# Kernel tuning notes

Measured on AMD Instinct MI355X. Metric: run time of the kernel, lower is better.

Reference implementation:

```python
import jax, jax.numpy as jnp
import numpy as np

B, T, R, D = 32, 128, 49, 512
H_EXP, H_CLS = 256, 256
THRES = 0.1
LAM = 4.0
NEG_INF = -1e9


def setup_inputs() -> dict:
    key = jax.random.key(0)
    ks = jax.random.split(key, 16)
    s = 0.02
    return {
        "word_emb": jax.random.normal(ks[0], (B, T, D), jnp.float32),
        "region_emb": jax.random.normal(ks[1], (B, R, D), jnp.float32),
        "attention_mask": jnp.ones((B, T), jnp.int32),
        # pos expert MLP: D -> H_EXP -> 1
        "pw1": jax.random.normal(ks[2], (D, H_EXP), jnp.float32) * s,
        "pb1": jnp.zeros((H_EXP,), jnp.float32),
        "pw2": jax.random.normal(ks[3], (H_EXP, 1), jnp.float32) * s,
        "pb2": jnp.zeros((1,), jnp.float32),
        # neg expert MLP: D -> H_EXP -> 1
        "nw1": jax.random.normal(ks[4], (D, H_EXP), jnp.float32) * s,
        "nb1": jnp.zeros((H_EXP,), jnp.float32),
        "nw2": jax.random.normal(ks[5], (H_EXP, 1), jnp.float32) * s,
        "nb2": jnp.zeros((1,), jnp.float32),
        # fc: D -> 1
        "fcw": jax.random.normal(ks[6], (D, 1), jnp.float32) * s,
        "fcb": jnp.zeros((1,), jnp.float32),
        # classifier: D -> H_CLS -> 2 (dropout is eval-mode identity)
        "cw1": jax.random.normal(ks[7], (D, H_CLS), jnp.float32) * s,
        "cb1": jnp.zeros((H_CLS,), jnp.float32),
        "cw2": jax.random.normal(ks[8], (H_CLS, 2), jnp.float32) * s,
        "cb2": jnp.zeros((2,), jnp.float32),
    }


def _mlp_score(x, w1, b1, w2, b2):
    # sigmoid(Linear(tanh(Linear(x)))) -> squeeze last dim
    return jax.nn.sigmoid(jnp.tanh(x @ w1 + b1) @ w2 + b2)[..., 0]


def reference(word_emb, region_emb, attention_mask,
              pw1, pb1, pw2, pb2, nw1, nb1, nw2, nb2,
              fcw, fcb, cw1, cb1, cw2, cb2):
    mask_f = attention_mask.astype(word_emb.dtype)  # [B,T]

    # cross attention word x region: [B,T,R]
    attn = jnp.einsum("btd,brd->btr", word_emb, region_emb)
    attn_neg = (attn - THRES > 0).astype(attn.dtype)  # [B,T,R]
    attn_pos = jax.nn.softmax(
        jnp.where(attn_neg > 0, attn, NEG_INF) * LAM, axis=-1)
    pos = jnp.einsum("btr,brd->btd", attn_pos, region_emb) + word_emb

    # pos expert: sigmoid score, zeroed where token has no positive region
    # or is padding (padding tokens were excluded by the ragged gather).
    expert_neg_mask = attn_neg.sum(-1) == 0  # [B,T] bool
    pos_score = _mlp_score(pos, pw1, pb1, pw2, pb2)  # [B,T]
    pos_score = jnp.where(expert_neg_mask, 0.0, pos_score) * mask_f
    pos_score = jax.nn.relu(pos_score)
    pos_agg = jnp.einsum("bt,btd->bd", pos_score, pos)

    # neg expert over all (token, region) pair embeddings, masked to the
    # ragged set neg_mask = (1 - attn_neg) * attention_mask
    all_emb = word_emb[:, :, None, :] + region_emb[:, None, :, :]  # [B,T,R,D]
    neg_mask = (1.0 - attn_neg) * mask_f[:, :, None]  # [B,T,R]
    neg_score = _mlp_score(all_emb, nw1, nb1, nw2, nb2)  # [B,T,R]
    neg_score = jax.nn.relu(neg_score * neg_mask)
    neg_agg = jnp.einsum("btr,btrd->bd", neg_score, all_emb)

    result = jnp.stack([neg_agg, pos_agg], axis=1)  # [B,2,D]

    choose = (result @ fcw + fcb)[..., 0]  # [B,2]
    choose_mask = attn_neg.sum(axis=(-1, -2)) == 0  # [B]
    choose = choose.at[:, 0].set(
        jnp.where(choose_mask, NEG_INF, choose[:, 0]))
    path_prob = jax.nn.softmax(choose, axis=-1)  # [B,2]
    final = jnp.einsum("bk,bkd->bd", path_prob, result)  # [B,D]

    logits = jax.nn.relu(final @ cw1 + cb1) @ cw2 + cb2  # [B,2]
    return (logits, path_prob)
```

## Files before the change

### kernel.cpp

```cpp
#include <hip/hip_runtime.h>

#define B_ 32
#define T_ 128
#define R_ 49
#define D_ 512
#define HE_ 256
#define HC_ 256

#define NG_GEMM1 354
#define NG_K1 512
#define NG_GEMM2 256
#define NG_NEGB 512

typedef float f32x4 __attribute__((ext_vector_type(4)));
typedef short s16x8 __attribute__((ext_vector_type(8)));
typedef short s16x4 __attribute__((ext_vector_type(4)));

__device__ __forceinline__ unsigned short bf16rne(float f) {
  unsigned u = __float_as_uint(f);
  u += 0x7FFF + ((u >> 16) & 1);
  return (unsigned short)(u >> 16);
}
__device__ __forceinline__ float rcp_fast(float x) {
  return __builtin_amdgcn_rcpf(x);
}
__device__ __forceinline__ float tanh_fast(float x) {
  float e = __expf(2.0f * x);
  return fmaf(-2.0f, rcp_fast(e + 1.0f), 1.0f);
}
__device__ __forceinline__ float sigmoid_fast(float x) {
  return rcp_fast(1.0f + __expf(-x));
}
__device__ __forceinline__ float wave_sum(float v) {
#pragma unroll
  for (int off = 32; off; off >>= 1) v += __shfl_down(v, off);
  return v;
}

__global__ __launch_bounds__(256) void pack_w(
    const float* __restrict__ nw1, const float* __restrict__ pw1,
    unsigned short* __restrict__ wp, float* __restrict__ nsr) {
  int gid = blockIdx.x * 256 + threadIdx.x;
  if (gid < B_ * R_) nsr[gid] = 0.f;
  int mat = gid >> 14;
  int rem = gid & 16383;
  int lane = rem & 63;
  int tile = rem >> 6;
  int kt = tile >> 4, ct = tile & 15;
  const float* W = mat ? pw1 : nw1;
  int k0 = kt * 32 + (lane >> 4) * 8;
  int c = ct * 16 + (lane & 15);
  s16x8 pk;
#pragma unroll
  for (int j = 0; j < 8; ++j)
    pk[j] = (short)bf16rne(W[(size_t)(k0 + j) * HE_ + c]);
  *(s16x8*)(wp + (size_t)gid * 8) = pk;
}

__global__ __launch_bounds__(512) void m1_gemm_k1(
    const float* __restrict__ word, const float* __restrict__ region,
    const unsigned short* __restrict__ wpack, const float* __restrict__ nb1,
    const int* __restrict__ amask, float* __restrict__ wh,
    float* __restrict__ rh, float* __restrict__ pos,
    float* __restrict__ negcnt, unsigned long long* __restrict__ nmask) {
  __shared__ alignas(16) unsigned short As[16 * 512];
  __shared__ float attn_s[8][52];
  __shared__ alignas(16) float wp_T[49][8];
  int tid = threadIdx.x, wave = tid >> 6, lane = tid & 63;
  int bid = blockIdx.x;

  if (bid < NG_GEMM1) {
    const float* A;
    float* outp;
    int row0;
    bool useb;
    if (bid < 256) {
      A = word; outp = wh; row0 = bid * 16; useb = true;
    } else {
      A = region; outp = rh; row0 = (bid - 256) * 16; useb = false;
    }
    const float4* A4 = (const float4*)(A + (size_t)row0 * D_);
#pragma unroll
    for (int it = 0; it < 4; ++it) {
      int f = it * 512 + tid;
      int row = f >> 7, kq = f & 127;
      float4 v = A4[f];
      int bo = (row * 1024 + kq * 8) ^ ((row & 7) << 4);
      s16x4 pk;
      pk[0] = (short)bf16rne(v.x);
      pk[1] = (short)bf16rne(v.y);
      pk[2] = (short)bf16rne(v.z);
      pk[3] = (short)bf16rne(v.w);
      *(s16x4*)((char*)As + bo) = pk;
    }
    __syncthreads();
    int rl = lane & 15, kg = lane >> 4;
    f32x4 acc0 = {0.f, 0.f, 0.f, 0.f}, acc1 = {0.f, 0.f, 0.f, 0.f};
    const s16x8* Wp8 = (const s16x8*)wpack;
    int ct0 = wave, ct1 = wave + 8;
#pragma unroll
    for (int kt = 0; kt < 16; ++kt) {
      int bo = (rl * 1024 + kt * 64 + kg * 16) ^ ((rl & 7) << 4);
      s16x8 af = *(const s16x8*)((char*)As + bo);
      s16x8 b0 = Wp8[(size_t)(kt * 16 + ct0) * 64 + lane];
      s16x8 b1 = Wp8[(size_t)(kt * 16 + ct1) * 64 + lane];
      acc0 = __builtin_amdgcn_mfma_f32_16x16x32_bf16(af, b0, acc0, 0, 0, 0);
      acc1 = __builtin_amdgcn_mfma_f32_16x16x32_bf16(af, b1, acc1, 0, 0, 0);
    }
    float bb0 = useb ? nb1[ct0 * 16 + rl] : 0.f;
    float bb1 = useb ? nb1[ct1 * 16 + rl] : 0.f;
    int r0 = row0 + kg * 4;
#pragma unroll
    for (int q = 0; q < 4; ++q) {
      outp[(size_t)(r0 + q) * HE_ + ct0 * 16 + rl] = acc0[q] + bb0;
      outp[(size_t)(r0 + q) * HE_ + ct1 * 16 + rl] = acc1[q] + bb1;
    }
    return;
  }

  int bid2 = bid - NG_GEMM1;
  int b = bid2 >> 4;
  int t0 = (bid2 & 15) * 8;
  int bt0 = b * T_ + t0;
  const float* reg = region + (size_t)b * R_ * D_;

  const float4* word4 = (const float4*)word;
  float4 wv[8][2];
#pragma unroll
  for (int t = 0; t < 8; ++t)
#pragma unroll
    for (int j = 0; j < 2; ++j)
      wv[t][j] = word4[(size_t)(bt0 + t) * 128 + lane * 2 + j];

  for (int r = wave; r < R_; r += 8) {
    const float4* rrow4 = (const float4*)(reg + (size_t)r * D_);
    float4 rv0 = rrow4[lane * 2 + 0];
    float4 rv1 = rrow4[lane * 2 + 1];
#pragma unroll
    for (int t = 0; t < 8; ++t) {
      float4 w0 = wv[t][0], w1 = wv[t][1];
      float acc = 0.f;
      acc = fmaf(w0.x, rv0.x, acc);
      acc = fmaf(w0.y, rv0.y, acc);
      acc = fmaf(w0.z, rv0.z, acc);
      acc = fmaf(w0.w, rv0.w, acc);
      acc = fmaf(w1.x, rv1.x, acc);
      acc = fmaf(w1.y, rv1.y, acc);
      acc = fmaf(w1.z, rv1.z, acc);
      acc = fmaf(w1.w, rv1.w, acc);
      acc = wave_sum(acc);
      if (lane == 0) attn_s[t][r] = acc;
    }
  }
  __syncthreads();

  {
    int t = wave;
    int am = amask[bt0 + t];
    float a = (lane < R_) ? attn_s[t][lane] : 0.f;
    float neg = (lane < R_ && (a - 0.1f) > 0.f) ? 1.f : 0.f;
    float masked = (lane < R_) ? ((neg > 0.f) ? a * 4.0f : -4e9f) : -3.0e38f;
    float cnt = wave_sum(neg);
    float m = masked;
#pragma unroll
    for (int off = 32; off; off >>= 1) m = fmaxf(m, __shfl_down(m, off));
    m = __shfl(m, 0);
    float e = (lane < R_) ? __expf(masked - m) : 0.f;
    float s = wave_sum(e);
    s = __shfl(s, 0);
    if (lane < R_) wp_T[lane][t] = e / s;
    bool want = (lane < R_) && (neg == 0.f) && (am != 0);
    unsigned long long bm = __ballot(want);
    if (lane == 0) {
      negcnt[bt0 + t] = cnt;
      nmask[bt0 + t] = bm;
    }
  }
  __syncthreads();

  int d = tid;
  float accs[8] = {0.f, 0.f, 0.f, 0.f, 0.f, 0.f, 0.f, 0.f};
#pragma unroll 7
  for (int r = 0; r < R_; ++r) {
    float g = reg[(size_t)r * D_ + d];
    float4 w0 = *(const float4*)&wp_T[r][0];
    float4 w1 = *(const float4*)&wp_T[r][4];
    accs[0] = fmaf(w0.x, g, accs[0]);
    accs[1] = fmaf(w0.y, g, accs[1]);
    accs[2] = fmaf(w0.z, g, accs[2]);
    accs[3] = fmaf(w0.w, g, accs[3]);
    accs[4] = fmaf(w1.x, g, accs[4]);
    accs[5] = fmaf(w1.y, g, accs[5]);
    accs[6] = fmaf(w1.z, g, accs[6]);
    accs[7] = fmaf(w1.w, g, accs[7]);
  }
#pragma unroll
  for (int t = 0; t < 8; ++t) {
    size_t base = (size_t)(bt0 + t) * D_ + d;
    pos[base] = word[base] + accs[t];
  }
}

__global__ __launch_bounds__(512) void m2_hps_neg(
    const float* __restrict__ pos, const unsigned short* __restrict__ wpack,
    const float* __restrict__ pb1, const float* __restrict__ pw2,
    const float* __restrict__ pb2, const float* __restrict__ negcnt,
    const int* __restrict__ amask, const float* __restrict__ wh,
    const float* __restrict__ rh, const float* __restrict__ nw2,
    const float* __restrict__ nb2,
    const unsigned long long* __restrict__ nmask,
    float* __restrict__ pscore, float* __restrict__ nst,
    float* __restrict__ nsr) {
  __shared__ union SM {
    struct G {
      alignas(16) unsigned short As[16 * 512];
      float sred[16][4];
    } g;
    struct N {
      alignas(16) float rh_s[R_ * HE_];
      alignas(16) float wh_s[8 * HE_];
      int plist[400];
      float nst_l[8];
      float nsr_l[52];
      int cnt_s[8];
      int off_s[8];
      int P;
    } n;
  } sm;
  int tid = threadIdx.x, wave = tid >> 6, lane = tid & 63;
  int bid = blockIdx.x;

  if (bid < NG_GEMM2) {
    int row0 = bid * 16;
    const float4* A4 = (const float4*)(pos + (size_t)row0 * D_);
#pragma unroll
    for (int it = 0; it < 4; ++it) {
      int f = it * 512 + tid;
      int row = f >> 7, kq = f & 127;
      float4 v = A4[f];
      int bo = (row * 1024 + kq * 8) ^ ((row & 7) << 4);
      s16x4 pk;
      pk[0] = (short)bf16rne(v.x);
      pk[1] = (short)bf16rne(v.y);
      pk[2] = (short)bf16rne(v.z);
      pk[3] = (short)bf16rne(v.w);
      *(s16x4*)((char*)sm.g.As + bo) = pk;
    }
    __syncthreads();
    int rl = lane & 15, kg = lane >> 4;
    f32x4 acc0 = {0.f, 0.f, 0.f, 0.f}, acc1 = {0.f, 0.f, 0.f, 0.f};
    const s16x8* Wp8 = (const s16x8*)wpack + 16384;
    int ct0 = wave, ct1 = wave + 8;
#pragma unroll
    for (int kt = 0; kt < 16; ++kt) {
      int bo = (rl * 1024 + kt * 64 + kg * 16) ^ ((rl & 7) << 4);
      s16x8 af = *(const s16x8*)((char*)sm.g.As + bo);
      s16x8 b0 = Wp8[(size_t)(kt * 16 + ct0) * 64 + lane];
      s16x8 b1 = Wp8[(size_t)(kt * 16 + ct1) * 64 + lane];
      acc0 = __builtin_amdgcn_mfma_f32_16x16x32_bf16(af, b0, acc0, 0, 0, 0);
      acc1 = __builtin_amdgcn_mfma_f32_16x16x32_bf16(af, b1, acc1, 0, 0, 0);
    }
    __syncthreads();
    float* hp_s = (float*)sm.g.As;
#pragma unroll
    for (int q = 0; q < 4; ++q) {
      hp_s[(kg * 4 + q) * 256 + ct0 * 16 + rl] = acc0[q];
      hp_s[(kg * 4 + q) * 256 + ct1 * 16 + rl] = acc1[q];
    }
    __syncthreads();
    int c = tid & 255, jh = tid >> 8;
    float pb1c = pb1[c], pw2c = pw2[c];
#pragma unroll
    for (int jj = 0; jj < 8; ++jj) {
      int j = jh * 8 + jj;
      float v = tanh_fast(hp_s[j * 256 + c] + pb1c) * pw2c;
      v = wave_sum(v);
      if (lane == 0) sm.g.sred[j][wave & 3] = v;
    }
    __syncthreads();
    if (tid < 16) {
      float s = sm.g.sred[tid][0] + sm.g.sred[tid][1] + sm.g.sred[tid][2] +
                sm.g.sred[tid][3] + pb2[0];
      s = sigmoid_fast(s);
      int row = row0 + tid;
      if (negcnt[row] == 0.f) s = 0.f;
      s *= (float)amask[row];
      pscore[row] = fmaxf(s, 0.f);
    }
    return;
  }

  int nb = bid - NG_GEMM2;
  int b = nb >> 4, t0 = (nb & 15) * 8;
  int bt0 = b * T_ + t0;
  {
    const float4* src = (const float4*)(rh + (size_t)b * R_ * HE_);
    float4* dst = (float4*)sm.n.rh_s;
    for (int i = tid; i < R_ * (HE_ / 4); i += 512) dst[i] = src[i];
    const float4* srcw = (const float4*)(wh + (size_t)bt0 * HE_);
    float4* dstw = (float4*)sm.n.wh_s;
    for (int i = tid; i < 8 * (HE_ / 4); i += 512) dstw[i] = srcw[i];
  }
  if (tid < 8) {
    sm.n.nst_l[tid] = 0.f;
    sm.n.cnt_s[tid] = __popcll(nmask[bt0 + tid]);
  }
  if (tid < R_) sm.n.nsr_l[tid] = 0.f;
  __syncthreads();
  if (tid == 0) {
    int tot = 0;
#pragma unroll
    for (int w = 0; w < 8; ++w) {
      sm.n.off_s[w] = tot;
      tot += sm.n.cnt_s[w];
    }
    sm.n.P = tot;
  }
  __syncthreads();
  {
    unsigned long long mw = nmask[bt0 + wave];
    if (lane < R_ && ((mw >> lane) & 1ull)) {
      int pfx = __popcll(mw & ((1ull << lane) - 1ull));
      sm.n.plist[sm.n.off_s[wave] + pfx] = (wave << 6) | lane;
    }
  }
  __syncthreads();
  int P = sm.n.P;
  int grp = tid >> 4, gl = tid & 15;
  float4 wnr[4];
#pragma unroll
  for (int k = 0; k < 4; ++k)
    wnr[k] = ((const float4*)nw2)[4 * gl + ((gl + k) & 3)];
  float bias = nb2[0];
  for (int i = grp; i < P; i += 32) {
    int tr = sm.n.plist[i];
    int t = tr >> 6, r = tr & 63;
    const float4* wrow = (const float4*)(sm.n.wh_s + t * HE_);
    const float4* rrow = (const float4*)(sm.n.rh_s + r * HE_);
    float acc = 0.f;
#pragma unroll
    for (int k = 0; k < 4; ++k) {
      int c = 4 * gl + ((gl + k) & 3);
      float4 hw = wrow[c];
      float4 hr = rrow[c];
      float4 wn = wnr[k];
      acc = fmaf(tanh_fast(hw.x + hr.x), wn.x, acc);
      acc = fmaf(tanh_fast(hw.y + hr.y), wn.y, acc);
      acc = fmaf(tanh_fast(hw.z + hr.z), wn.z, acc);
      acc = fmaf(tanh_fast(hw.w + hr.w), wn.w, acc);
    }
    acc += __shfl_xor(acc, 1);
    acc += __shfl_xor(acc, 2);
    acc += __shfl_xor(acc, 4);
    acc += __shfl_xor(acc, 8);
    if (gl == 0) {
      float s = sigmoid_fast(acc + bias);
      atomicAdd(&sm.n.nst_l[t], s);
      atomicAdd(&sm.n.nsr_l[r], s);
    }
  }
  __syncthreads();
  if (tid < 8) {
    nst[bt0 + tid] = sm.n.nst_l[tid];
  } else if (tid >= 64 && tid < 64 + R_) {
    atomicAdd(&nsr[b * R_ + (tid - 64)], sm.n.nsr_l[tid - 64]);
  }
}

__global__ __launch_bounds__(512) void k7a_agg(
    const float* __restrict__ word, const float* __restrict__ region,
    const float* __restrict__ pos, const float* __restrict__ pscore,
    const float* __restrict__ nst, const float* __restrict__ nsr,
    float* __restrict__ nagg, float* __restrict__ pagg) {
  int b = blockIdx.x >> 3, dc = blockIdx.x & 7;
  int tid = threadIdx.x;
  int dl = tid & 63, ts = tid >> 6;
  int d = dc * 64 + dl;
  __shared__ float nst_s[T_], psc_s[T_], nsr_s[R_];
  __shared__ float redn[8][64], redp[8][64];
  if (tid < T_) {
    psc_s[tid] = pscore[b * T_ + tid];
    nst_s[tid] = nst[b * T_ + tid];
  } else if (tid < T_ + R_) {
    nsr_s[tid - T_] = nsr[b * R_ + (tid - T_)];
  }
  __syncthreads();
  float na = 0.f, pa = 0.f;
  for (int t = ts; t < T_; t += 8) {
    size_t base = ((size_t)(b * T_ + t)) * D_ + d;
    na = fmaf(nst_s[t], word[base], na);
    pa = fmaf(psc_s[t], pos[base], pa);
  }
  for (int r = ts; r < R_; r += 8)
    na = fmaf(nsr_s[r], region[((size_t)(b * R_ + r)) * D_ + d], na);
  redn[ts][dl] = na;
  redp[ts][dl] = pa;
  __syncthreads();
  if (tid < 64) {
    float s = 0.f;
#pragma unroll
    for (int k = 0; k < 8; ++k) s += redn[k][tid];
    nagg[(size_t)b * D_ + dc * 64 + tid] = s;
  } else if (tid < 128) {
    int l = tid - 64;
    float s = 0.f;
#pragma unroll
    for (int k = 0; k < 8; ++k) s += redp[k][l];
    pagg[(size_t)b * D_ + dc * 64 + l] = s;
  }
}

__global__ __launch_bounds__(256) void k7b_tail(
    const float* __restrict__ nagg, const float* __restrict__ pagg,
    const float* __restrict__ negcnt, const float* __restrict__ fcw,
    const float* __restrict__ fcb, const float* __restrict__ cw1,
    const float* __restrict__ cb1, const float* __restrict__ cw2,
    const float* __restrict__ cb2, float* __restrict__ out) {
  int b = blockIdx.x, tid = threadIdx.x, lane = tid & 63, wave = tid >> 6;
  __shared__ float na_s[D_], pa_s[D_], fin[D_];
  __shared__ float red[8];
  __shared__ float pp0, pp1;
  float cntp = (tid < T_) ? negcnt[b * T_ + tid] : 0.f;
  float cw = wave_sum(cntp);
  if (lane == 0) red[wave] = cw;
  int d0 = tid, d1 = tid + 256;
  float n0 = nagg[(size_t)b * D_ + d0], n1 = nagg[(size_t)b * D_ + d1];
  float p0 = pagg[(size_t)b * D_ + d0], p1 = pagg[(size_t)b * D_ + d1];
  na_s[d0] = n0;
  na_s[d1] = n1;
  pa_s[d0] = p0;
  pa_s[d1] = p1;
  __syncthreads();
  float cnt_total = red[0] + red[1] + red[2] + red[3];
  float f0 = fcw[d0], f1 = fcw[d1];
  float c0p = n0 * f0 + n1 * f1;
  float c1p = p0 * f0 + p1 * f1;
  c0p = wave_sum(c0p);
  c1p = wave_sum(c1p);
  __syncthreads();
  if (lane == 0) { red[wave] = c0p; red[wave + 4] = c1p; }
  __syncthreads();
  if (tid == 0) {
    float c0 = red[0] + red[1] + red[2] + red[3] + fcb[0];
    float c1 = red[4] + red[5] + red[6] + red[7] + fcb[0];
    if (cnt_total == 0.f) c0 = -1e9f;
    float m = fmaxf(c0, c1);
    float e0 = __expf(c0 - m), e1 = __expf(c1 - m);
    float inv = 1.f / (e0 + e1);
    pp0 = e0 * inv;
    pp1 = e1 * inv;
    out[2 * B_ + 2 * b + 0] = pp0;
    out[2 * B_ + 2 * b + 1] = pp1;
  }
  __syncthreads();
  for (int d = tid; d < D_; d += 256) fin[d] = pp0 * na_s[d] + pp1 * pa_s[d];
  __syncthreads();
  float a0 = cb1[tid], a1 = 0.f, a2 = 0.f, a3 = 0.f;
#pragma unroll 4
  for (int d = 0; d < D_; d += 4) {
    a0 = fmaf(fin[d + 0], cw1[(size_t)(d + 0) * HC_ + tid], a0);
    a1 = fmaf(fin[d + 1], cw1[(size_t)(d + 1) * HC_ + tid], a1);
    a2 = fmaf(fin[d + 2], cw1[(size_t)(d + 2) * HC_ + tid], a2);
    a3 = fmaf(fin[d + 3], cw1[(size_t)(d + 3) * HC_ + tid], a3);
  }
  float acc = fmaxf((a0 + a1) + (a2 + a3), 0.f);
  float l0 = acc * cw2[2 * tid + 0];
  float l1 = acc * cw2[2 * tid + 1];
  l0 = wave_sum(l0);
  l1 = wave_sum(l1);
  __syncthreads();
  if (lane == 0) { red[wave] = l0; red[wave + 4] = l1; }
  __syncthreads();
  if (tid == 0) {
    out[2 * b + 0] = red[0] + red[1] + red[2] + red[3] + cb2[0];
    out[2 * b + 1] = red[4] + red[5] + red[6] + red[7] + cb2[1];
  }
}

extern "C" void kernel_launch(void* const* d_in, const int* in_sizes, int n_in,
                              void* d_out, int out_size, void* d_ws,
                              size_t ws_size, hipStream_t stream) {
  const float* word = (const float*)d_in[0];
  const float* region = (const float*)d_in[1];
  const int* amask = (const int*)d_in[2];
  const float* pw1 = (const float*)d_in[3];
  const float* pb1 = (const float*)d_in[4];
  const float* pw2 = (const float*)d_in[5];
  const float* pb2 = (const float*)d_in[6];
  const float* nw1 = (const float*)d_in[7];
  const float* nb1 = (const float*)d_in[8];
  const float* nw2 = (const float*)d_in[9];
  const float* nb2 = (const float*)d_in[10];
  const float* fcw = (const float*)d_in[11];
  const float* fcb = (const float*)d_in[12];
  const float* cw1 = (const float*)d_in[13];
  const float* cb1 = (const float*)d_in[14];
  const float* cw2 = (const float*)d_in[15];
  const float* cb2 = (const float*)d_in[16];
  float* out = (float*)d_out;

  unsigned short* wpack = (unsigned short*)d_ws;
  float* ws = (float*)d_ws + 131072;
  float* pos = ws;
  float* wh = pos + (size_t)B_ * T_ * D_;
  float* rh = wh + (size_t)B_ * T_ * HE_;
  float* nst = rh + (size_t)B_ * R_ * HE_;
  float* nsr = nst + (size_t)B_ * T_;
  float* negcnt = nsr + (size_t)B_ * R_;
  float* pscore = negcnt + B_ * T_;
  float* nagg = pscore + B_ * T_;
  float* pagg = nagg + (size_t)B_ * D_;
  unsigned long long* nmask =
      (unsigned long long*)(pagg + (size_t)B_ * D_);

  pack_w<<<128, 256, 0, stream>>>(nw1, pw1, wpack, nsr);
  m1_gemm_k1<<<NG_GEMM1 + NG_K1, 512, 0, stream>>>(
      word, region, wpack, nb1, amask, wh, rh, pos, negcnt, nmask);
  m2_hps_neg<<<NG_GEMM2 + NG_NEGB, 512, 0, stream>>>(
      pos, wpack, pb1, pw2, pb2, negcnt, amask, wh, rh, nw2, nb2, nmask,
      pscore, nst, nsr);
  k7a_agg<<<B_ * 8, 512, 0, stream>>>(word, region, pos, pscore, nst, nsr,
                                      nagg, pagg);
  k7b_tail<<<B_, 256, 0, stream>>>(nagg, pagg, negcnt, fcw, fcb, cw1, cb1,
                                   cw2, cb2, out);
}
```

Measured before the change: 85.05 us.

## Regroup kernel stages: fuse weight packing with attention, merge all GEMMs

Weight packing moves into the attention kernel as extra blocks, so there is one fewer launch. The word/region GEMMs move out of that kernel and join the pos-expert GEMM in a single gemm_all launch. The neg-expert scoring becomes its own kernel with smaller shared memory: wh rows are no longer staged and are read directly from global, and a launch-bounds hint is added. The attention loop now processes tokens in two passes of 4 to lower register pressure. The kernel count stays the same, but the dependency grouping changes, and the neg expert now reads wh from global memory instead of LDS.

```diff
diff --git a/kernel.cpp b/kernel.cpp
--- a/kernel.cpp
+++ b/kernel.cpp
@@ -7,9 +7,10 @@
 #define HE_ 256
 #define HC_ 256
 
-#define NG_GEMM1 354
+#define NG_PACK 64
 #define NG_K1 512
-#define NG_GEMM2 256
+#define NG_G1 354
+#define NG_G2 256
 #define NG_NEGB 512
 
 typedef float f32x4 __attribute__((ext_vector_type(4)));
@@ -37,119 +38,71 @@
   return v;
 }
 
-__global__ __launch_bounds__(256) void pack_w(
+__global__ __launch_bounds__(512, 8) void k1_pack(
+    const float* __restrict__ word, const float* __restrict__ region,
     const float* __restrict__ nw1, const float* __restrict__ pw1,
-    unsigned short* __restrict__ wp, float* __restrict__ nsr) {
-  int gid = blockIdx.x * 256 + threadIdx.x;
-  if (gid < B_ * R_) nsr[gid] = 0.f;
-  int mat = gid >> 14;
-  int rem = gid & 16383;
-  int lane = rem & 63;
-  int tile = rem >> 6;
-  int kt = tile >> 4, ct = tile & 15;
-  const float* W = mat ? pw1 : nw1;
-  int k0 = kt * 32 + (lane >> 4) * 8;
-  int c = ct * 16 + (lane & 15);
-  s16x8 pk;
-#pragma unroll
-  for (int j = 0; j < 8; ++j)
-    pk[j] = (short)bf16rne(W[(size_t)(k0 + j) * HE_ + c]);
-  *(s16x8*)(wp + (size_t)gid * 8) = pk;
-}
-
-__global__ __launch_bounds__(512) void m1_gemm_k1(
-    const float* __restrict__ word, const float* __restrict__ region,
-    const unsigned short* __restrict__ wpack, const float* __restrict__ nb1,
-    const int* __restrict__ amask, float* __restrict__ wh,
-    float* __restrict__ rh, float* __restrict__ pos,
+    const int* __restrict__ amask, unsigned short* __restrict__ wp,
+    float* __restrict__ nsr, float* __restrict__ pos,
     float* __restrict__ negcnt, unsigned long long* __restrict__ nmask) {
-  __shared__ alignas(16) unsigned short As[16 * 512];
   __shared__ float attn_s[8][52];
   __shared__ alignas(16) float wp_T[49][8];
   int tid = threadIdx.x, wave = tid >> 6, lane = tid & 63;
   int bid = blockIdx.x;
 
-  if (bid < NG_GEMM1) {
-    const float* A;
-    float* outp;
-    int row0;
-    bool useb;
-    if (bid < 256) {
-      A = word; outp = wh; row0 = bid * 16; useb = true;
-    } else {
-      A = region; outp = rh; row0 = (bid - 256) * 16; useb = false;
-    }
-    const float4* A4 = (const float4*)(A + (size_t)row0 * D_);
-#pragma unroll
-    for (int it = 0; it < 4; ++it) {
-      int f = it * 512 + tid;
-      int row = f >> 7, kq = f & 127;
-      float4 v = A4[f];
-      int bo = (row * 1024 + kq * 8) ^ ((row & 7) << 4);
-      s16x4 pk;
-      pk[0] = (short)bf16rne(v.x);
-      pk[1] = (short)bf16rne(v.y);
-      pk[2] = (short)bf16rne(v.z);
-      pk[3] = (short)bf16rne(v.w);
-      *(s16x4*)((char*)As + bo) = pk;
-    }
-    __syncthreads();
-    int rl = lane & 15, kg = lane >> 4;
-    f32x4 acc0 = {0.f, 0.f, 0.f, 0.f}, acc1 = {0.f, 0.f, 0.f, 0.f};
-    const s16x8* Wp8 = (const s16x8*)wpack;
-    int ct0 = wave, ct1 = wave + 8;
-#pragma unroll
-    for (int kt = 0; kt < 16; ++kt) {
-      int bo = (rl * 1024 + kt * 64 + kg * 16) ^ ((rl & 7) << 4);
-      s16x8 af = *(const s16x8*)((char*)As + bo);
-      s16x8 b0 = Wp8[(size_t)(kt * 16 + ct0) * 64 + lane];
-      s16x8 b1 = Wp8[(size_t)(kt * 16 + ct1) * 64 + lane];
-      acc0 = __builtin_amdgcn_mfma_f32_16x16x32_bf16(af, b0, acc0, 0, 0, 0);
-      acc1 = __builtin_amdgcn_mfma_f32_16x16x32_bf16(af, b1, acc1, 0, 0, 0);
-    }
-    float bb0 = useb ? nb1[ct0 * 16 + rl] : 0.f;
-    float bb1 = useb ? nb1[ct1 * 16 + rl] : 0.f;
-    int r0 = row0 + kg * 4;
-#pragma unroll
-    for (int q = 0; q < 4; ++q) {
-      outp[(size_t)(r0 + q) * HE_ + ct0 * 16 + rl] = acc0[q] + bb0;
-      outp[(size_t)(r0 + q) * HE_ + ct1 * 16 + rl] = acc1[q] + bb1;
-    }
+  if (bid < NG_PACK) {
+    int gid = bid * 512 + tid;
+    if (gid < B_ * R_) nsr[gid] = 0.f;
+    int mat = gid >> 14;
+    int rem = gid & 16383;
+    int plane = rem & 63;
+    int tile = rem >> 6;
+    int kt = tile >> 4, ct = tile & 15;
+    const float* W = mat ? pw1 : nw1;
+    int k0 = kt * 32 + (plane >> 4) * 8;
+    int c = ct * 16 + (plane & 15);
+    s16x8 pk;
+#pragma unroll
+    for (int j = 0; j < 8; ++j)
+      pk[j] = (short)bf16rne(W[(size_t)(k0 + j) * HE_ + c]);
+    *(s16x8*)(wp + (size_t)gid * 8) = pk;
     return;
   }
 
-  int bid2 = bid - NG_GEMM1;
+  int bid2 = bid - NG_PACK;
   int b = bid2 >> 4;
   int t0 = (bid2 & 15) * 8;
   int bt0 = b * T_ + t0;
   const float* reg = region + (size_t)b * R_ * D_;
-
   const float4* word4 = (const float4*)word;
-  float4 wv[8][2];
-#pragma unroll
-  for (int t = 0; t < 8; ++t)
-#pragma unroll
-    for (int j = 0; j < 2; ++j)
-      wv[t][j] = word4[(size_t)(bt0 + t) * 128 + lane * 2 + j];
-
-  for (int r = wave; r < R_; r += 8) {
-    const float4* rrow4 = (const float4*)(reg + (size_t)r * D_);
-    float4 rv0 = rrow4[lane * 2 + 0];
-    float4 rv1 = rrow4[lane * 2 + 1];
-#pragma unroll
-    for (int t = 0; t < 8; ++t) {
-      float4 w0 = wv[t][0], w1 = wv[t][1];
-      float acc = 0.f;
-      acc = fmaf(w0.x, rv0.x, acc);
-      acc = fmaf(w0.y, rv0.y, acc);
-      acc = fmaf(w0.z, rv0.z, acc);
-      acc = fmaf(w0.w, rv0.w, acc);
-      acc = fmaf(w1.x, rv1.x, acc);
-      acc = fmaf(w1.y, rv1.y, acc);
-      acc = fmaf(w1.z, rv1.z, acc);
-      acc = fmaf(w1.w, rv1.w, acc);
-      acc = wave_sum(acc);
-      if (lane == 0) attn_s[t][r] = acc;
+
+#pragma unroll
+  for (int pass = 0; pass < 2; ++pass) {
+    int tp = pass * 4;
+    float4 wv[4][2];
+#pragma unroll
+    for (int t = 0; t < 4; ++t)
+#pragma unroll
+      for (int j = 0; j < 2; ++j)
+        wv[t][j] = word4[(size_t)(bt0 + tp + t) * 128 + lane * 2 + j];
+    for (int r = wave; r < R_; r += 8) {
+      const float4* rrow4 = (const float4*)(reg + (size_t)r * D_);
+      float4 rv0 = rrow4[lane * 2 + 0];
+      float4 rv1 = rrow4[lane * 2 + 1];
+#pragma unroll
+      for (int t = 0; t < 4; ++t) {
+        float4 w0 = wv[t][0], w1 = wv[t][1];
+        float acc = 0.f;
+        acc = fmaf(w0.x, rv0.x, acc);
+        acc = fmaf(w0.y, rv0.y, acc);
+        acc = fmaf(w0.z, rv0.z, acc);
+        acc = fmaf(w0.w, rv0.w, acc);
+        acc = fmaf(w1.x, rv1.x, acc);
+        acc = fmaf(w1.y, rv1.y, acc);
+        acc = fmaf(w1.z, rv1.z, acc);
+        acc = fmaf(w1.w, rv1.w, acc);
+        acc = wave_sum(acc);
+        if (lane == 0) attn_s[tp + t][r] = acc;
+      }
     }
   }
   __syncthreads();
@@ -201,131 +154,149 @@
   }
 }
 
-__global__ __launch_bounds__(512) void m2_hps_neg(
+__global__ __launch_bounds__(512) void gemm_all(
+    const float* __restrict__ word, const float* __restrict__ region,
     const float* __restrict__ pos, const unsigned short* __restrict__ wpack,
-    const float* __restrict__ pb1, const float* __restrict__ pw2,
-    const float* __restrict__ pb2, const float* __restrict__ negcnt,
-    const int* __restrict__ amask, const float* __restrict__ wh,
-    const float* __restrict__ rh, const float* __restrict__ nw2,
-    const float* __restrict__ nb2,
-    const unsigned long long* __restrict__ nmask,
-    float* __restrict__ pscore, float* __restrict__ nst,
-    float* __restrict__ nsr) {
-  __shared__ union SM {
-    struct G {
-      alignas(16) unsigned short As[16 * 512];
-      float sred[16][4];
-    } g;
-    struct N {
-      alignas(16) float rh_s[R_ * HE_];
-      alignas(16) float wh_s[8 * HE_];
-      int plist[400];
-      float nst_l[8];
-      float nsr_l[52];
-      int cnt_s[8];
-      int off_s[8];
-      int P;
-    } n;
-  } sm;
+    const float* __restrict__ nb1, const float* __restrict__ pb1,
+    const float* __restrict__ pw2, const float* __restrict__ pb2,
+    const float* __restrict__ negcnt, const int* __restrict__ amask,
+    float* __restrict__ wh, float* __restrict__ rh,
+    float* __restrict__ pscore) {
+  __shared__ alignas(16) unsigned short As[16 * 512];
+  __shared__ float sred[16][4];
   int tid = threadIdx.x, wave = tid >> 6, lane = tid & 63;
   int bid = blockIdx.x;
 
-  if (bid < NG_GEMM2) {
-    int row0 = bid * 16;
-    const float4* A4 = (const float4*)(pos + (size_t)row0 * D_);
-#pragma unroll
-    for (int it = 0; it < 4; ++it) {
-      int f = it * 512 + tid;
-      int row = f >> 7, kq = f & 127;
-      float4 v = A4[f];
-      int bo = (row * 1024 + kq * 8) ^ ((row & 7) << 4);
-      s16x4 pk;
-      pk[0] = (short)bf16rne(v.x);
-      pk[1] = (short)bf16rne(v.y);
-      pk[2] = (short)bf16rne(v.z);
-      pk[3] = (short)bf16rne(v.w);
-      *(s16x4*)((char*)sm.g.As + bo) = pk;
-    }
-    __syncthreads();
-    int rl = lane & 15, kg = lane >> 4;
-    f32x4 acc0 = {0.f, 0.f, 0.f, 0.f}, acc1 = {0.f, 0.f, 0.f, 0.f};
-    const s16x8* Wp8 = (const s16x8*)wpack + 16384;
-    int ct0 = wave, ct1 = wave + 8;
-#pragma unroll
-    for (int kt = 0; kt < 16; ++kt) {
-      int bo = (rl * 1024 + kt * 64 + kg * 16) ^ ((rl & 7) << 4);
-      s16x8 af = *(const s16x8*)((char*)sm.g.As + bo);
-      s16x8 b0 = Wp8[(size_t)(kt * 16 + ct0) * 64 + lane];
-      s16x8 b1 = Wp8[(size_t)(kt * 16 + ct1) * 64 + lane];
-      acc0 = __builtin_amdgcn_mfma_f32_16x16x32_bf16(af, b0, acc0, 0, 0, 0);
-      acc1 = __builtin_amdgcn_mfma_f32_16x16x32_bf16(af, b1, acc1, 0, 0, 0);
-    }
-    __syncthreads();
-    float* hp_s = (float*)sm.g.As;
+  bool isg2 = (bid >= NG_G1);
+  const float* A;
+  float* outp = nullptr;
+  int row0;
+  bool useb = false;
+  const s16x8* Wp8;
+  if (!isg2) {
+    if (bid < 256) {
+      A = word; outp = wh; row0 = bid * 16; useb = true;
+    } else {
+      A = region; outp = rh; row0 = (bid - 256) * 16;
+    }
+    Wp8 = (const s16x8*)wpack;
+  } else {
+    A = pos; row0 = (bid - NG_G1) * 16;
+    Wp8 = (const s16x8*)wpack + 16384;
+  }
+  const float4* A4 = (const float4*)(A + (size_t)row0 * D_);
+#pragma unroll
+  for (int it = 0; it < 4; ++it) {
+    int f = it * 512 + tid;
+    int row = f >> 7, kq = f & 127;
+    float4 v = A4[f];
+    int bo = (row * 1024 + kq * 8) ^ ((row & 7) << 4);
+    s16x4 pk;
+    pk[0] = (short)bf16rne(v.x);
+    pk[1] = (short)bf16rne(v.y);
+    pk[2] = (short)bf16rne(v.z);
+    pk[3] = (short)bf16rne(v.w);
+    *(s16x4*)((char*)As + bo) = pk;
+  }
+  __syncthreads();
+  int rl = lane & 15, kg = lane >> 4;
+  f32x4 acc0 = {0.f, 0.f, 0.f, 0.f}, acc1 = {0.f, 0.f, 0.f, 0.f};
+  int ct0 = wave, ct1 = wave + 8;
+#pragma unroll
+  for (int kt = 0; kt < 16; ++kt) {
+    int bo = (rl * 1024 + kt * 64 + kg * 16) ^ ((rl & 7) << 4);
+    s16x8 af = *(const s16x8*)((char*)As + bo);
+    s16x8 b0 = Wp8[(size_t)(kt * 16 + ct0) * 64 + lane];
+    s16x8 b1 = Wp8[(size_t)(kt * 16 + ct1) * 64 + lane];
+    acc0 = __builtin_amdgcn_mfma_f32_16x16x32_bf16(af, b0, acc0, 0, 0, 0);
+    acc1 = __builtin_amdgcn_mfma_f32_16x16x32_bf16(af, b1, acc1, 0, 0, 0);
+  }
+  if (!isg2) {
+    float bb0 = useb ? nb1[ct0 * 16 + rl] : 0.f;
+    float bb1 = useb ? nb1[ct1 * 16 + rl] : 0.f;
+    int r0 = row0 + kg * 4;
 #pragma unroll
     for (int q = 0; q < 4; ++q) {
-      hp_s[(kg * 4 + q) * 256 + ct0 * 16 + rl] = acc0[q];
-      hp_s[(kg * 4 + q) * 256 + ct1 * 16 + rl] = acc1[q];
-    }
-    __syncthreads();
-    int c = tid & 255, jh = tid >> 8;
-    float pb1c = pb1[c], pw2c = pw2[c];
-#pragma unroll
-    for (int jj = 0; jj < 8; ++jj) {
-      int j = jh * 8 + jj;
-      float v = tanh_fast(hp_s[j * 256 + c] + pb1c) * pw2c;
-      v = wave_sum(v);
-      if (lane == 0) sm.g.sred[j][wave & 3] = v;
-    }
-    __syncthreads();
-    if (tid < 16) {
-      float s = sm.g.sred[tid][0] + sm.g.sred[tid][1] + sm.g.sred[tid][2] +
-                sm.g.sred[tid][3] + pb2[0];
-      s = sigmoid_fast(s);
-      int row = row0 + tid;
-      if (negcnt[row] == 0.f) s = 0.f;
-      s *= (float)amask[row];
-      pscore[row] = fmaxf(s, 0.f);
+      outp[(size_t)(r0 + q) * HE_ + ct0 * 16 + rl] = acc0[q] + bb0;
+      outp[(size_t)(r0 + q) * HE_ + ct1 * 16 + rl] = acc1[q] + bb1;
     }
     return;
   }
-
-  int nb = bid - NG_GEMM2;
+  __syncthreads();
+  float* hp_s = (float*)As;
+#pragma unroll
+  for (int q = 0; q < 4; ++q) {
+    hp_s[(kg * 4 + q) * 256 + ct0 * 16 + rl] = acc0[q];
+    hp_s[(kg * 4 + q) * 256 + ct1 * 16 + rl] = acc1[q];
+  }
+  __syncthreads();
+  int c = tid & 255, jh = tid >> 8;
+  float pb1c = pb1[c], pw2c = pw2[c];
+#pragma unroll
+  for (int jj = 0; jj < 8; ++jj) {
+    int j = jh * 8 + jj;
+    float v = tanh_fast(hp_s[j * 256 + c] + pb1c) * pw2c;
+    v = wave_sum(v);
+    if (lane == 0) sred[j][wave & 3] = v;
+  }
+  __syncthreads();
+  if (tid < 16) {
+    float s = sred[tid][0] + sred[tid][1] + sred[tid][2] + sred[tid][3] +
+              pb2[0];
+    s = sigmoid_fast(s);
+    int row = row0 + tid;
+    if (negcnt[row] == 0.f) s = 0.f;
+    s *= (float)amask[row];
+    pscore[row] = fmaxf(s, 0.f);
+  }
+}
+
+__global__ __launch_bounds__(512, 6) void neg_expert(
+    const float* __restrict__ wh, const float* __restrict__ rh,
+    const float* __restrict__ nw2, const float* __restrict__ nb2,
+    const unsigned long long* __restrict__ nmask, float* __restrict__ nst,
+    float* __restrict__ nsr) {
+  __shared__ alignas(16) float rh_s[R_ * HE_];
+  __shared__ int plist[400];
+  __shared__ float nst_l[8];
+  __shared__ float nsr_l[52];
+  __shared__ int cnt_s[8];
+  __shared__ int off_s[8];
+  __shared__ int P_s;
+  int tid = threadIdx.x, wave = tid >> 6, lane = tid & 63;
+  int nb = blockIdx.x;
   int b = nb >> 4, t0 = (nb & 15) * 8;
   int bt0 = b * T_ + t0;
   {
     const float4* src = (const float4*)(rh + (size_t)b * R_ * HE_);
-    float4* dst = (float4*)sm.n.rh_s;
+    float4* dst = (float4*)rh_s;
     for (int i = tid; i < R_ * (HE_ / 4); i += 512) dst[i] = src[i];
-    const float4* srcw = (const float4*)(wh + (size_t)bt0 * HE_);
-    float4* dstw = (float4*)sm.n.wh_s;
-    for (int i = tid; i < 8 * (HE_ / 4); i += 512) dstw[i] = srcw[i];
   }
   if (tid < 8) {
-    sm.n.nst_l[tid] = 0.f;
-    sm.n.cnt_s[tid] = __popcll(nmask[bt0 + tid]);
-  }
-  if (tid < R_) sm.n.nsr_l[tid] = 0.f;
+    nst_l[tid] = 0.f;
+    cnt_s[tid] = __popcll(nmask[bt0 + tid]);
+  }
+  if (tid < R_) nsr_l[tid] = 0.f;
   __syncthreads();
   if (tid == 0) {
     int tot = 0;
 #pragma unroll
     for (int w = 0; w < 8; ++w) {
-      sm.n.off_s[w] = tot;
-      tot += sm.n.cnt_s[w];
-    }
-    sm.n.P = tot;
+      off_s[w] = tot;
+      tot += cnt_s[w];
+    }
+    P_s = tot;
   }
   __syncthreads();
   {
     unsigned long long mw = nmask[bt0 + wave];
     if (lane < R_ && ((mw >> lane) & 1ull)) {
       int pfx = __popcll(mw & ((1ull << lane) - 1ull));
-      sm.n.plist[sm.n.off_s[wave] + pfx] = (wave << 6) | lane;
-    }
-  }
-  __syncthreads();
-  int P = sm.n.P;
+      plist[off_s[wave] + pfx] = (wave << 6) | lane;
+    }
+  }
+  __syncthreads();
+  int P = P_s;
   int grp = tid >> 4, gl = tid & 15;
   float4 wnr[4];
 #pragma unroll
@@ -333,10 +304,10 @@
     wnr[k] = ((const float4*)nw2)[4 * gl + ((gl + k) & 3)];
   float bias = nb2[0];
   for (int i = grp; i < P; i += 32) {
-    int tr = sm.n.plist[i];
+    int tr = plist[i];
     int t = tr >> 6, r = tr & 63;
-    const float4* wrow = (const float4*)(sm.n.wh_s + t * HE_);
-    const float4* rrow = (const float4*)(sm.n.rh_s + r * HE_);
+    const float4* wrow = (const float4*)(wh + (size_t)(bt0 + t) * HE_);
+    const float4* rrow = (const float4*)(rh_s + r * HE_);
     float acc = 0.f;
 #pragma unroll
     for (int k = 0; k < 4; ++k) {
@@ -355,15 +326,15 @@
     acc += __shfl_xor(acc, 8);
     if (gl == 0) {
       float s = sigmoid_fast(acc + bias);
-      atomicAdd(&sm.n.nst_l[t], s);
-      atomicAdd(&sm.n.nsr_l[r], s);
+      atomicAdd(&nst_l[t], s);
+      atomicAdd(&nsr_l[r], s);
     }
   }
   __syncthreads();
   if (tid < 8) {
-    nst[bt0 + tid] = sm.n.nst_l[tid];
+    nst[bt0 + tid] = nst_l[tid];
   } else if (tid >= 64 && tid < 64 + R_) {
-    atomicAdd(&nsr[b * R_ + (tid - 64)], sm.n.nsr_l[tid - 64]);
+    atomicAdd(&nsr[b * R_ + (tid - 64)], nsr_l[tid - 64]);
   }
 }
 
@@ -513,12 +484,12 @@
   unsigned long long* nmask =
       (unsigned long long*)(pagg + (size_t)B_ * D_);
 
-  pack_w<<<128, 256, 0, stream>>>(nw1, pw1, wpack, nsr);
-  m1_gemm_k1<<<NG_GEMM1 + NG_K1, 512, 0, stream>>>(
-      word, region, wpack, nb1, amask, wh, rh, pos, negcnt, nmask);
-  m2_hps_neg<<<NG_GEMM2 + NG_NEGB, 512, 0, stream>>>(
-      pos, wpack, pb1, pw2, pb2, negcnt, amask, wh, rh, nw2, nb2, nmask,
-      pscore, nst, nsr);
+  k1_pack<<<NG_PACK + NG_K1, 512, 0, stream>>>(
+      word, region, nw1, pw1, amask, wpack, nsr, pos, negcnt, nmask);
+  gemm_all<<<NG_G1 + NG_G2, 512, 0, stream>>>(
+      word, region, pos, wpack, nb1, pb1, pw2, pb2, negcnt, amask, wh, rh,
+      pscore);
+  neg_expert<<<NG_NEGB, 512, 0, stream>>>(wh, rh, nw2, nb2, nmask, nst, nsr);
   k7a_agg<<<B_ * 8, 512, 0, stream>>>(word, region, pos, pscore, nst, nsr,
                                       nagg, pagg);
   k7b_tail<<<B_, 256, 0, stream>>>(nagg, pagg, negcnt, fcw, fcb, cw1, cb1,
```

After: 85.13 us. No clear change (+0.1%).
